# Optimization experiments

Measured on AMD Instinct MI355X. Metric: run time of the kernel, lower is better.

## Reference

```python
import jax, jax.numpy as jnp
import numpy as np


def setup_inputs() -> dict:
    key = jax.random.key(0)
    ks = jax.random.split(key, 8)
    T, D = 8192, 36
    return {
        "embeddings": jax.random.normal(ks[0], (T, D), dtype=jnp.float32),
        "WQ_prog": jax.random.normal(ks[1], (2, D), dtype=jnp.float32),
        "WK_prog": jax.random.normal(ks[2], (2, D), dtype=jnp.float32),
        "WV_op": jax.random.normal(ks[3], (1, D), dtype=jnp.float32),
        "WV_arg": jax.random.normal(ks[4], (1, D), dtype=jnp.float32),
        "WQ_stack": jax.random.normal(ks[5], (2, D), dtype=jnp.float32),
        "WK_stack": jax.random.normal(ks[6], (2, D), dtype=jnp.float32),
        "WV_stack": jax.random.normal(ks[7], (1, D), dtype=jnp.float32),
    }


def reference(embeddings, WQ_prog, WK_prog, WV_op, WV_arg, WQ_stack, WK_stack, WV_stack):
    # --- program-fetch head: hard-argmax attention ---
    Q_prog = embeddings @ WQ_prog.T          # (T, 2)
    K_prog = embeddings @ WK_prog.T          # (T, 2)
    V_op = embeddings @ WV_op.T              # (T, 1)
    V_arg = embeddings @ WV_arg.T            # (T, 1)
    scores_prog = Q_prog @ K_prog.T          # (T, T)
    best_prog = jnp.argmax(scores_prog, axis=1)   # (T,)
    fetched_ops = V_op[best_prog, 0]
    fetched_args = V_arg[best_prog, 0]

    # --- stack-fetch head: hard-argmax attention ---
    Q_stack = embeddings @ WQ_stack.T        # (T, 2)
    K_stack = embeddings @ WK_stack.T        # (T, 2)
    V_stack = embeddings @ WV_stack.T        # (T, 1)
    scores_stack = Q_stack @ K_stack.T       # (T, T)
    best_stack = jnp.argmax(scores_stack, axis=1)
    fetched_vals = V_stack[best_stack, 0]

    return (fetched_ops, fetched_args, fetched_vals)
```

## Files before the change

### kernel.cpp

```cpp
#include <hip/hip_runtime.h>
#include <math.h>

#define T 8192
#define D 36
#define NCH 64
#define CHUNK (T / NCH)
#define RPT 8
#define ROWS_PER_BLOCK (256 * RPT)
#define RBLK (T / ROWS_PER_BLOCK)


__device__ __forceinline__ void load_row(const float* __restrict__ E, int j,
                                         float* e) {
    const float4* Er = (const float4*)(E + j * D);
#pragma unroll
    for (int i = 0; i < D / 4; ++i) {
        float4 v = Er[i];
        e[4 * i + 0] = v.x;
        e[4 * i + 1] = v.y;
        e[4 * i + 2] = v.z;
        e[4 * i + 3] = v.w;
    }
}

__global__ __launch_bounds__(256) void proj_qk(
    const float* __restrict__ E,
    const float* __restrict__ WQp, const float* __restrict__ WKp,
    const float* __restrict__ WQs, const float* __restrict__ WKs,
    float2* __restrict__ Qg, float2* __restrict__ Kg) {
    const int t = blockIdx.x * 256 + threadIdx.x;
    float e[D];
    load_row(E, t, e);
    float qp0 = 0.f, qp1 = 0.f, kp0 = 0.f, kp1 = 0.f;
    float qs0 = 0.f, qs1 = 0.f, ks0 = 0.f, ks1 = 0.f;
#pragma unroll
    for (int d = 0; d < D; ++d) {
        float ed = e[d];
        qp0 = fmaf(ed, WQp[d], qp0);
        qp1 = fmaf(ed, WQp[D + d], qp1);
        kp0 = fmaf(ed, WKp[d], kp0);
        kp1 = fmaf(ed, WKp[D + d], kp1);
        qs0 = fmaf(ed, WQs[d], qs0);
        qs1 = fmaf(ed, WQs[D + d], qs1);
        ks0 = fmaf(ed, WKs[d], ks0);
        ks1 = fmaf(ed, WKs[D + d], ks1);
    }
    Qg[t] = make_float2(qp0, qp1);
    Qg[T + t] = make_float2(qs0, qs1);
    Kg[t] = make_float2(kp0, kp1);
    Kg[T + t] = make_float2(ks0, ks1);
}

__global__ __launch_bounds__(256) void maxscan(
    const float2* __restrict__ Qg, const float2* __restrict__ Kg,
    float* __restrict__ pv) {
    const int head = blockIdx.z;
    const int row0 = blockIdx.x * ROWS_PER_BLOCK;
    const int j0 = blockIdx.y * CHUNK;

    __shared__ float4 sk4[CHUNK / 2];
    if (threadIdx.x < CHUNK)
        ((float2*)sk4)[threadIdx.x] = Kg[head * T + j0 + threadIdx.x];

    float2 q[RPT];
#pragma unroll
    for (int i = 0; i < RPT; ++i)
        q[i] = Qg[head * T + row0 + i * 256 + threadIdx.x];
    __syncthreads();

    float best[RPT];
#pragma unroll
    for (int i = 0; i < RPT; ++i) best[i] = -INFINITY;

#pragma unroll 8
    for (int k = 0; k < CHUNK / 2; ++k) {
        float4 kk = sk4[k];
#pragma unroll
        for (int i = 0; i < RPT; ++i) {
            float s0 = fmaf(q[i].x, kk.x, q[i].y * kk.y);
            float s1 = fmaf(q[i].x, kk.z, q[i].y * kk.w);
            best[i] = fmaxf(best[i], fmaxf(s0, s1));
        }
    }
    const int base = blockIdx.y * 2 * T + head * T + row0 + threadIdx.x;
#pragma unroll
    for (int i = 0; i < RPT; ++i) pv[base + i * 256] = best[i];
}

__global__ __launch_bounds__(256) void finalize(
    const float* __restrict__ E,
    const float* __restrict__ WVop, const float* __restrict__ WVarg,
    const float* __restrict__ WVs,
    const float* __restrict__ pv, const float2* __restrict__ Qg,
    const float2* __restrict__ Kg, float* __restrict__ out) {
    const int wid = threadIdx.x >> 6;
    const int lane = threadIdx.x & 63;
    const int prow = blockIdx.x * 4 + wid;
    const int head = prow >> 13;
    const int row = prow & (T - 1);

    const float v = pv[lane * 2 * T + prow];
    float m = v;
#pragma unroll
    for (int off = 32; off; off >>= 1) m = fmaxf(m, __shfl_xor(m, off));
    const unsigned long long cb = __ballot(v == m);
    const int cwin = __ffsll(cb) - 1;

    const float2 q = Qg[prow];
    int bi;
    {
        int j = head * T + cwin * CHUNK + lane;
        float2 kk = Kg[j];
        float s = fmaf(q.x, kk.x, q.y * kk.y);
        unsigned long long eb = __ballot(s == m);
        if (eb) {
            bi = cwin * CHUNK + __ffsll(eb) - 1;
        } else {
            kk = Kg[j + 64];
            s = fmaf(q.x, kk.x, q.y * kk.y);
            eb = __ballot(s == m);
            bi = cwin * CHUNK + 64 + __ffsll(eb) - 1;
        }
    }

    float e[D];
    load_row(E, bi, e);
    if (head == 0) {
        float vop = 0.f, varg = 0.f;
#pragma unroll
        for (int d = 0; d < D; ++d) {
            vop = fmaf(e[d], WVop[d], vop);
            varg = fmaf(e[d], WVarg[d], varg);
        }
        if (lane == 0) {
            out[row] = vop;
            out[T + row] = varg;
        }
    } else {
        float vs = 0.f;
#pragma unroll
        for (int d = 0; d < D; ++d) vs = fmaf(e[d], WVs[d], vs);
        if (lane == 0) out[2 * T + row] = vs;
    }
}

extern "C" void kernel_launch(void* const* d_in, const int* in_sizes, int n_in,
                              void* d_out, int out_size, void* d_ws,
                              size_t ws_size, hipStream_t stream) {
    const float* E = (const float*)d_in[0];
    const float* WQp = (const float*)d_in[1];
    const float* WKp = (const float*)d_in[2];
    const float* WVop = (const float*)d_in[3];
    const float* WVarg = (const float*)d_in[4];
    const float* WQs = (const float*)d_in[5];
    const float* WKs = (const float*)d_in[6];
    const float* WVs = (const float*)d_in[7];
    float* out = (float*)d_out;

    float* wsf = (float*)d_ws;
    float* pv = wsf;
    float2* Kg = (float2*)(wsf + 2 * T * NCH);
    float2* Qg = (float2*)(wsf + 2 * T * NCH + 4 * T);

    proj_qk<<<T / 256, 256, 0, stream>>>(E, WQp, WKp, WQs, WKs, Qg, Kg);

    dim3 gB(RBLK, NCH, 2);
    maxscan<<<gB, 256, 0, stream>>>(Qg, Kg, pv);

    finalize<<<(2 * T) / 4, 256, 0, stream>>>(E, WVop, WVarg, WVs, pv, Qg, Kg,
                                              out);
}
```

Before: 94.31 us.

## Fuse Q/K projection into max-scan kernel, recomputing projections per block

Removes the separate projection kernel and has each scan block compute its own K chunk and Q rows directly from the embeddings. Designated blocks still write Q and K to the workspace for the finalize pass. This saves one kernel launch and the inter-kernel dependency, but every block now recomputes Q projections (64x redundancy across chunks) and K projections (4x across row blocks). It also re-reads embeddings many times, relying on cache.

```diff
diff --git a/kernel.cpp b/kernel.cpp
--- a/kernel.cpp
+++ b/kernel.cpp
@@ -23,55 +23,60 @@
     }
 }
 
-__global__ __launch_bounds__(256) void proj_qk(
+__global__ __launch_bounds__(256) void scanfused(
     const float* __restrict__ E,
     const float* __restrict__ WQp, const float* __restrict__ WKp,
     const float* __restrict__ WQs, const float* __restrict__ WKs,
-    float2* __restrict__ Qg, float2* __restrict__ Kg) {
-    const int t = blockIdx.x * 256 + threadIdx.x;
-    float e[D];
-    load_row(E, t, e);
-    float qp0 = 0.f, qp1 = 0.f, kp0 = 0.f, kp1 = 0.f;
-    float qs0 = 0.f, qs1 = 0.f, ks0 = 0.f, ks1 = 0.f;
-#pragma unroll
-    for (int d = 0; d < D; ++d) {
-        float ed = e[d];
-        qp0 = fmaf(ed, WQp[d], qp0);
-        qp1 = fmaf(ed, WQp[D + d], qp1);
-        kp0 = fmaf(ed, WKp[d], kp0);
-        kp1 = fmaf(ed, WKp[D + d], kp1);
-        qs0 = fmaf(ed, WQs[d], qs0);
-        qs1 = fmaf(ed, WQs[D + d], qs1);
-        ks0 = fmaf(ed, WKs[d], ks0);
-        ks1 = fmaf(ed, WKs[D + d], ks1);
-    }
-    Qg[t] = make_float2(qp0, qp1);
-    Qg[T + t] = make_float2(qs0, qs1);
-    Kg[t] = make_float2(kp0, kp1);
-    Kg[T + t] = make_float2(ks0, ks1);
-}
+    float* __restrict__ pv, float2* __restrict__ Kg, float2* __restrict__ Qg) {
+    const int head = blockIdx.z;
+    const float* __restrict__ WQ = head ? WQs : WQp;
+    const float* __restrict__ WK = head ? WKs : WKp;
 
-__global__ __launch_bounds__(256) void maxscan(
-    const float2* __restrict__ Qg, const float2* __restrict__ Kg,
-    float* __restrict__ pv) {
-    const int head = blockIdx.z;
-    const int row0 = blockIdx.x * ROWS_PER_BLOCK;
+    __shared__ float2 sk[CHUNK];
     const int j0 = blockIdx.y * CHUNK;
 
-    __shared__ float4 sk4[CHUNK / 2];
-    if (threadIdx.x < CHUNK)
-        ((float2*)sk4)[threadIdx.x] = Kg[head * T + j0 + threadIdx.x];
+    if (threadIdx.x < CHUNK) {
+        const int j = j0 + threadIdx.x;
+        float e[D];
+        load_row(E, j, e);
+        float k0 = 0.f, k1 = 0.f;
+#pragma unroll
+        for (int d = 0; d < D; ++d) {
+            k0 = fmaf(e[d], WK[d], k0);
+            k1 = fmaf(e[d], WK[D + d], k1);
+        }
+        float2 kk = make_float2(k0, k1);
+        sk[threadIdx.x] = kk;
+        if (blockIdx.x == 0) Kg[head * T + j] = kk;
+    }
 
+    const int row0 = blockIdx.x * ROWS_PER_BLOCK;
     float2 q[RPT];
 #pragma unroll
-    for (int i = 0; i < RPT; ++i)
-        q[i] = Qg[head * T + row0 + i * 256 + threadIdx.x];
+    for (int i = 0; i < RPT; ++i) {
+        const int row = row0 + i * 256 + threadIdx.x;
+        float e[D];
+        load_row(E, row, e);
+        float q0 = 0.f, q1 = 0.f;
+#pragma unroll
+        for (int d = 0; d < D; ++d) {
+            q0 = fmaf(e[d], WQ[d], q0);
+            q1 = fmaf(e[d], WQ[D + d], q1);
+        }
+        q[i] = make_float2(q0, q1);
+    }
+    if (blockIdx.y == 0) {
+#pragma unroll
+        for (int i = 0; i < RPT; ++i)
+            Qg[head * T + row0 + i * 256 + threadIdx.x] = q[i];
+    }
     __syncthreads();
 
     float best[RPT];
 #pragma unroll
     for (int i = 0; i < RPT; ++i) best[i] = -INFINITY;
 
+    const float4* sk4 = (const float4*)sk;
 #pragma unroll 8
     for (int k = 0; k < CHUNK / 2; ++k) {
         float4 kk = sk4[k];
@@ -162,10 +167,8 @@
     float2* Kg = (float2*)(wsf + 2 * T * NCH);
     float2* Qg = (float2*)(wsf + 2 * T * NCH + 4 * T);
 
-    proj_qk<<<T / 256, 256, 0, stream>>>(E, WQp, WKp, WQs, WKs, Qg, Kg);
-
-    dim3 gB(RBLK, NCH, 2);
-    maxscan<<<gB, 256, 0, stream>>>(Qg, Kg, pv);
+    dim3 gA(RBLK, NCH, 2);
+    scanfused<<<gA, 256, 0, stream>>>(E, WQp, WKp, WQs, WKs, pv, Kg, Qg);
 
     finalize<<<(2 * T) / 4, 256, 0, stream>>>(E, WVop, WVarg, WVs, pv, Qg, Kg,
                                               out);
```

After: 114.5 us. 21.4% more time.
